# Optimization experiments

Hardware: AMD Instinct MI355X
Metric: run time of the kernel (lower is better)

The kernel has to match this reference:

```python
import jax, jax.numpy as jnp
import numpy as np

# ---- pywt filter banks (dec_lo, dec_hi, rec_lo, rec_hi), all pywt-ordered ----
_SQ2 = 0.7071067811865476

def _orth(dec_lo):
    dec_lo = np.asarray(dec_lo, dtype=np.float64)
    rec_lo = dec_lo[::-1].copy()
    k = np.arange(len(dec_lo))
    dec_hi = ((-1.0) ** (k + 1)) * rec_lo
    rec_hi = dec_hi[::-1].copy()
    return dec_lo, dec_hi, rec_lo, rec_hi

_DB4 = [-0.010597401784997278, 0.032883011666982945, 0.030841381835986965,
        -0.18703481171888114, -0.02798376941698385, 0.6308807679295904,
        0.7148465705525415, 0.23037781330885523]
_SYM6 = [-0.007800708325034148, 0.0017677118642428036, 0.04472490177066578,
         -0.021060292512300564, -0.07263752278646252, 0.3379294217276218,
         0.787641141030194, 0.4910559419267466, -0.048311742585633,
         -0.11799011114819057, 0.0034907120842174702, 0.015404109327027373]
_BIOR13 = (
    np.array([-0.08838834764831845, 0.08838834764831845, _SQ2, _SQ2, 0.08838834764831845, -0.08838834764831845]),
    np.array([0.0, 0.0, -_SQ2, _SQ2, 0.0, 0.0]),
    np.array([0.0, 0.0, _SQ2, _SQ2, 0.0, 0.0]),
    np.array([-0.08838834764831845, -0.08838834764831845, _SQ2, -_SQ2, 0.08838834764831845, 0.08838834764831845]),
)

WAVELETS = ['haar', 'db4', 'sym6', 'bior1.3']
FILTERS = {
    'haar': _orth([_SQ2, _SQ2]),
    'db4': _orth(_DB4),
    'sym6': _orth(_SYM6),
    'bior1.3': _BIOR13,
}
FILTERS = {k: tuple(jnp.asarray(f, dtype=jnp.float32) for f in v) for k, v in FILTERS.items()}


def _dwt(x, dec_lo, dec_hi):
    # x: [B, C, T] (T even). ptwt: reflect-pad (2L-3)//2 each side, stride-2 corr with flipped dec filters.
    B, C, T = x.shape
    L = dec_lo.shape[0]
    p = (2 * L - 3) // 2
    xp = jnp.pad(x, ((0, 0), (0, 0), (p, p)), mode='reflect') if p > 0 else x
    filt = jnp.stack([dec_lo[::-1], dec_hi[::-1]])[:, None, :].astype(x.dtype)  # [2,1,L]
    out = jax.lax.conv_general_dilated(
        xp.reshape(B * C, 1, -1), filt, window_strides=(2,), padding='VALID',
        dimension_numbers=('NCH', 'OIH', 'NCH'))
    out = out.reshape(B, C, 2, -1)
    return out[:, :, 0], out[:, :, 1]  # approx, detail: [B, C, (T+L-2)//2]


def _idwt(lo, hi, rec_lo, rec_hi):
    # conv_transpose stride 2 with rec filters, then crop (2L-3)//2 per side (ptwt waverec).
    B, C, Tc = lo.shape
    L = rec_lo.shape[0]
    p = (2 * L - 3) // 2
    c = jnp.stack([lo, hi], axis=2).reshape(B * C, 2, Tc)
    filt = jnp.stack([rec_lo[::-1], rec_hi[::-1]])[None].astype(lo.dtype)  # [1,2,L]
    y = jax.lax.conv_general_dilated(
        c, filt, window_strides=(1,), padding=[(L - 1, L - 1)],
        lhs_dilation=(2,), dimension_numbers=('NCH', 'OIH', 'NCH'))
    y = y.reshape(B, C, -1)
    if p > 0:
        y = y[:, :, p:-p]
    return y


def _spectral(z, lam, gamma, cos_theta):
    return gamma * jnp.sign(z) * jax.nn.relu(jnp.abs(z) - lam) * cos_theta


def setup_inputs() -> dict:
    key = jax.random.key(0)
    ks = jax.random.split(key, 8)
    B, S, E = 8, 4096, 1024
    x = jax.random.normal(ks[0], (B, S, E), dtype=jnp.float32)
    lambda_approx = jnp.full((1, E, 1), 0.05, jnp.float32) + 0.01 * jax.random.uniform(ks[1], (1, E, 1), jnp.float32)
    lambda_detail = jnp.full((1, E, 1), 0.05, jnp.float32) + 0.01 * jax.random.uniform(ks[2], (1, E, 1), jnp.float32)
    log_gamma = 0.1 * jax.random.normal(ks[3], (1, E, 1), jnp.float32)
    theta = 0.1 * jax.random.normal(ks[4], (1, E, 1), jnp.float32)
    basis_logits = 0.5 * jax.random.normal(ks[5], (4,), jnp.float32)
    ln_weight = jnp.ones((E,), jnp.float32)
    ln_bias = jnp.zeros((E,), jnp.float32)
    return {'x': x, 'lambda_approx': lambda_approx, 'lambda_detail': lambda_detail,
            'log_gamma': log_gamma, 'theta': theta, 'basis_logits': basis_logits,
            'ln_weight': ln_weight, 'ln_bias': ln_bias}


def reference(x, lambda_approx, lambda_detail, log_gamma, theta, basis_logits, ln_weight, ln_bias):
    residual = x                       # [B, S, E]
    S = x.shape[1]
    xt = jnp.transpose(x, (0, 2, 1))   # [B, E, S]
    gamma = jax.nn.softplus(log_gamma) + 1e-6
    ct = jnp.cos(theta)
    weights = jax.nn.softmax(basis_logits)  # all 4 wavelets valid for even S
    out = jnp.zeros_like(xt)
    for i, name in enumerate(WAVELETS):
        dl, dh, rl, rh = FILTERS[name]
        lo, hi = _dwt(xt, dl, dh)
        lo = _spectral(lo, lambda_approx, gamma, ct)
        hi = _spectral(hi, lambda_detail, gamma, ct)
        rec = _idwt(lo, hi, rl, rh)[:, :, :S]
        out = out + weights[i] * rec
    y = jnp.transpose(out, (0, 2, 1)) + residual
    mu = jnp.mean(y, axis=-1, keepdims=True)
    var = jnp.var(y, axis=-1, keepdims=True)
    return (y - mu) / jnp.sqrt(var + 1e-5) * ln_weight + ln_bias
```

## Files before the change

### kernel.cpp

```cpp
#include <hip/hip_runtime.h>
#include <cstdint>

#define T_SEQ 4096
#define E_DIM 1024
#define N_B   8
#define SC    64
typedef float v2f __attribute__((ext_vector_type(2)));

constexpr int LW[4] = {2, 8, 12, 6};

constexpr float DLf[4][12] = {
  {0.7071067811865476f, 0.7071067811865476f, 0,0,0,0,0,0,0,0,0,0},
  {-0.010597401784997278f, 0.032883011666982945f, 0.030841381835986965f, -0.18703481171888114f,
   -0.02798376941698385f, 0.6308807679295904f, 0.7148465705525415f, 0.23037781330885523f, 0,0,0,0},
  {-0.007800708325034148f, 0.0017677118642428036f, 0.04472490177066578f, -0.021060292512300564f,
   -0.07263752278646252f, 0.3379294217276218f, 0.787641141030194f, 0.4910559419267466f,
   -0.048311742585633f, -0.11799011114819057f, 0.0034907120842174702f, 0.015404109327027373f},
  {-0.08838834764831845f, 0.08838834764831845f, 0.7071067811865476f, 0.7071067811865476f,
    0.08838834764831845f, -0.08838834764831845f, 0,0,0,0,0,0},
};
constexpr float DHf[4][12] = {
  {-0.7071067811865476f, 0.7071067811865476f, 0,0,0,0,0,0,0,0,0,0},
  {-0.23037781330885523f, 0.7148465705525415f, -0.6308807679295904f, -0.02798376941698385f,
    0.18703481171888114f, 0.030841381835986965f, -0.032883011666982945f, -0.010597401784997278f, 0,0,0,0},
  {-0.015404109327027373f, 0.0034907120842174702f, 0.11799011114819057f, -0.048311742585633f,
   -0.4910559419267466f, 0.787641141030194f, -0.3379294217276218f, -0.07263752278646252f,
    0.021060292512300564f, 0.04472490177066578f, -0.0017677118642428036f, -0.007800708325034148f},
  {0,0,-0.7071067811865476f, 0.7071067811865476f, 0,0, 0,0,0,0,0,0},
};
constexpr float RLf[4][12] = {
  {0.7071067811865476f, 0.7071067811865476f, 0,0,0,0,0,0,0,0,0,0},
  {0.23037781330885523f, 0.7148465705525415f, 0.6308807679295904f, -0.02798376941698385f,
   -0.18703481171888114f, 0.030841381835986965f, 0.032883011666982945f, -0.010597401784997278f, 0,0,0,0},
  {0.015404109327027373f, 0.0034907120842174702f, -0.11799011114819057f, -0.048311742585633f,
   0.4910559419267466f, 0.787641141030194f, 0.3379294217276218f, -0.07263752278646252f,
   -0.021060292512300564f, 0.04472490177066578f, 0.0017677118642428036f, -0.007800708325034148f},
  {0,0,0.7071067811865476f, 0.7071067811865476f, 0,0, 0,0,0,0,0,0},
};
constexpr float RHf[4][12] = {
  {0.7071067811865476f, -0.7071067811865476f, 0,0,0,0,0,0,0,0,0,0},
  {-0.010597401784997278f, -0.032883011666982945f, 0.030841381835986965f, 0.18703481171888114f,
   -0.02798376941698385f, -0.6308807679295904f, 0.7148465705525415f, -0.23037781330885523f, 0,0,0,0},
  {-0.007800708325034148f, -0.0017677118642428036f, 0.04472490177066578f, 0.021060292512300564f,
   -0.07263752278646252f, -0.3379294217276218f, 0.787641141030194f, -0.4910559419267466f,
   -0.048311742585633f, 0.11799011114819057f, 0.0034907120842174702f, -0.015404109327027373f},
  {-0.08838834764831845f, -0.08838834764831845f, 0.7071067811865476f, -0.7071067811865476f,
    0.08838834764831845f, 0.08838834764831845f, 0,0,0,0,0,0},
};

__device__ __forceinline__ v2f sv(float c) { return v2f{c, c}; }

template <int W, int KK>
__device__ __forceinline__ void step(const v2f (&xw)[36], v2f (&acc)[16],
                                     const v2f la, const v2f ld, const v2f gw) {
  constexpr int L = LW[W];
  if constexpr (KK < L / 2 + 7) {
    v2f lo = {0.f, 0.f}, hi = {0.f, 0.f};
#pragma unroll
    for (int m = 0; m < L; ++m) {
      const v2f xv = xw[2 * KK + 11 - m];
      if (DLf[W][m] != 0.0f) lo += sv(DLf[W][m]) * xv;
      if (DHf[W][m] != 0.0f) hi += sv(DHf[W][m]) * xv;
    }
    v2f cl, ch;
    cl.x = __builtin_amdgcn_fmed3f(lo.x, -la.x, la.x);
    cl.y = __builtin_amdgcn_fmed3f(lo.y, -la.y, la.y);
    ch.x = __builtin_amdgcn_fmed3f(hi.x, -ld.x, ld.x);
    ch.y = __builtin_amdgcn_fmed3f(hi.y, -ld.y, ld.y);
    const v2f loS = (lo - cl) * gw;
    const v2f hiS = (hi - ch) * gw;
#pragma unroll
    for (int m = 0; m < L; ++m) {
      const int j = 2 * KK + m + 2 - L;
      if (j >= 0 && j < 16) {
        if (RLf[W][m] != 0.0f) acc[j] += loS * sv(RLf[W][m]);
        if (RHf[W][m] != 0.0f) acc[j] += hiS * sv(RHf[W][m]);
      }
    }
  }
}

template <int KK>
__device__ __forceinline__ void sweep(const v2f (&xw)[36], v2f (&acc)[16],
                                      const v2f la, const v2f ld,
                                      const v2f gw0, const v2f gw1,
                                      const v2f gw2, const v2f gw3) {
  if constexpr (KK < 13) {
    step<0, KK>(xw, acc, la, ld, gw0);
    step<1, KK>(xw, acc, la, ld, gw1);
    step<2, KK>(xw, acc, la, ld, gw2);
    step<3, KK>(xw, acc, la, ld, gw3);
    if constexpr (KK < 8) {
      acc[2 * KK]     += xw[2 * KK + 10];
      acc[2 * KK + 1] += xw[2 * KK + 11];
    }
    sweep<KK + 1>(xw, acc, la, ld, gw0, gw1, gw2, gw3);
  }
}

__global__ __launch_bounds__(256) void wlm_k1(
    const float* __restrict__ x,
    const float* __restrict__ la_, const float* __restrict__ ld_,
    const float* __restrict__ lg_, const float* __restrict__ th_,
    const float* __restrict__ bl_, float* __restrict__ y) {
  const int tid  = threadIdx.x;
  const int lane = tid & 63;
  const int wave = tid >> 6;
  const int s0 = blockIdx.x * SC;
  const int e0 = blockIdx.y * 128;
  const int b  = blockIdx.z;
  const int e  = e0 + 2 * lane;
  const int sA = s0 + wave * 16;

  const size_t rowb = (size_t)b * T_SEQ;
  v2f xw[36];
  if (sA >= 10 && sA + 26 <= T_SEQ) {
    const float* p = &x[(rowb + sA - 10) * E_DIM + e];
#pragma unroll
    for (int i = 0; i < 36; ++i) {
      xw[i] = *reinterpret_cast<const v2f*>(p + (size_t)i * E_DIM);
    }
  } else {
#pragma unroll
    for (int i = 0; i < 36; ++i) {
      int g = sA - 10 + i;
      g = (g < 0) ? -g : g;
      g = (g >= T_SEQ) ? (2 * T_SEQ - 2 - g) : g;
      xw[i] = *reinterpret_cast<const v2f*>(&x[(rowb + g) * E_DIM + e]);
    }
  }

  const v2f la = *reinterpret_cast<const v2f*>(&la_[e]);
  const v2f ld = *reinterpret_cast<const v2f*>(&ld_[e]);
  const v2f lg = *reinterpret_cast<const v2f*>(&lg_[e]);
  const v2f th = *reinterpret_cast<const v2f*>(&th_[e]);
  v2f g2;
  g2.x = (fmaxf(lg.x, 0.f) + log1pf(expf(-fabsf(lg.x))) + 1e-6f) * cosf(th.x);
  g2.y = (fmaxf(lg.y, 0.f) + log1pf(expf(-fabsf(lg.y))) + 1e-6f) * cosf(th.y);

  const float b0 = bl_[0], b1 = bl_[1], b2 = bl_[2], b3 = bl_[3];
  const float mx = fmaxf(fmaxf(b0, b1), fmaxf(b2, b3));
  const float w0 = expf(b0 - mx), w1 = expf(b1 - mx),
              w2 = expf(b2 - mx), w3 = expf(b3 - mx);
  const float wr = 1.f / (w0 + w1 + w2 + w3);
  const v2f gw0 = g2 * sv(w0 * wr), gw1 = g2 * sv(w1 * wr),
            gw2 = g2 * sv(w2 * wr), gw3 = g2 * sv(w3 * wr);

  v2f acc[16];
#pragma unroll
  for (int j = 0; j < 16; ++j) acc[j] = v2f{0.f, 0.f};

  sweep<0>(xw, acc, la, ld, gw0, gw1, gw2, gw3);

#pragma unroll
  for (int j = 0; j < 16; ++j) {
    *reinterpret_cast<v2f*>(&y[(rowb + sA + j) * E_DIM + e]) = acc[j];
  }
}

__global__ __launch_bounds__(256) void wlm_k2(float* __restrict__ y,
                                              const float* __restrict__ w,
                                              const float* __restrict__ bias) {
  const int token = blockIdx.x;
  const int tid = threadIdx.x;
  float* row = y + (size_t)token * E_DIM;

  float4 v = *reinterpret_cast<const float4*>(&row[tid * 4]);
  float s  = v.x + v.y + v.z + v.w;
  float sq = v.x * v.x + v.y * v.y + v.z * v.z + v.w * v.w;
#pragma unroll
  for (int off = 32; off; off >>= 1) {
    s  += __shfl_down(s, off);
    sq += __shfl_down(sq, off);
  }
  __shared__ float ps[4], pq[4], stat[2];
  const int wave = tid >> 6, lane = tid & 63;
  if (lane == 0) { ps[wave] = s; pq[wave] = sq; }
  __syncthreads();
  if (tid == 0) {
    const float S1 = ps[0] + ps[1] + ps[2] + ps[3];
    const float S2 = pq[0] + pq[1] + pq[2] + pq[3];
    const float mu = S1 * (1.f / E_DIM);
    const float var = S2 * (1.f / E_DIM) - mu * mu;
    stat[0] = mu;
    stat[1] = rsqrtf(var + 1e-5f);
  }
  __syncthreads();
  const float mu = stat[0], rstd = stat[1];
  const float4 wv = *reinterpret_cast<const float4*>(&w[tid * 4]);
  const float4 bv = *reinterpret_cast<const float4*>(&bias[tid * 4]);
  float4 o;
  o.x = (v.x - mu) * rstd * wv.x + bv.x;
  o.y = (v.y - mu) * rstd * wv.y + bv.y;
  o.z = (v.z - mu) * rstd * wv.z + bv.z;
  o.w = (v.w - mu) * rstd * wv.w + bv.w;
  *reinterpret_cast<float4*>(&row[tid * 4]) = o;
}

extern "C" void kernel_launch(void* const* d_in, const int* in_sizes, int n_in,
                              void* d_out, int out_size, void* d_ws, size_t ws_size,
                              hipStream_t stream) {
  const float* x   = (const float*)d_in[0];
  const float* la  = (const float*)d_in[1];
  const float* ldt = (const float*)d_in[2];
  const float* lg  = (const float*)d_in[3];
  const float* th  = (const float*)d_in[4];
  const float* bl  = (const float*)d_in[5];
  const float* lnw = (const float*)d_in[6];
  const float* lnb = (const float*)d_in[7];
  float* out = (float*)d_out;

  dim3 g1(T_SEQ / SC, E_DIM / 128, N_B);
  wlm_k1<<<g1, 256, 0, stream>>>(x, la, ldt, lg, th, bl, out);
  wlm_k2<<<dim3(N_B * T_SEQ), 256, 0, stream>>>(out, lnw, lnb);
}
```

Baseline: 111.9 us.

## Fuse wavelet filtering and LayerNorm into one kernel with full-row blocks

Merges the wavelet filter kernel and the LayerNorm kernel into a single kernel. Each 512-thread block now covers all 1024 channels for 16 consecutive tokens, so per-row mean and variance are reduced in-block through shuffles and shared memory. This removes the intermediate write and re-read of the full output tensor and one kernel launch. In exchange, the grid shrinks to 2048 blocks, the x halo is re-read per 16-token tile, and 16 serial per-row reductions are added per thread.

```diff
diff --git a/kernel.cpp b/kernel.cpp
--- a/kernel.cpp
+++ b/kernel.cpp
@@ -4,7 +4,7 @@
 #define T_SEQ 4096
 #define E_DIM 1024
 #define N_B   8
-#define SC    64
+#define BT    16
 typedef float v2f __attribute__((ext_vector_type(2)));
 
 constexpr int LW[4] = {2, 8, 12, 6};
@@ -98,19 +98,21 @@
   }
 }
 
-__global__ __launch_bounds__(256) void wlm_k1(
+__global__ __launch_bounds__(512) void wlm_fused(
     const float* __restrict__ x,
     const float* __restrict__ la_, const float* __restrict__ ld_,
     const float* __restrict__ lg_, const float* __restrict__ th_,
-    const float* __restrict__ bl_, float* __restrict__ y) {
+    const float* __restrict__ bl_,
+    const float* __restrict__ lnw, const float* __restrict__ lnb,
+    float* __restrict__ y) {
+  __shared__ float ps[BT][8], pq[BT][8], stat[BT][2];
+
   const int tid  = threadIdx.x;
   const int lane = tid & 63;
   const int wave = tid >> 6;
-  const int s0 = blockIdx.x * SC;
-  const int e0 = blockIdx.y * 128;
+  const int e  = 2 * tid;
   const int b  = blockIdx.z;
-  const int e  = e0 + 2 * lane;
-  const int sA = s0 + wave * 16;
+  const int sA = blockIdx.x * BT;
 
   const size_t rowb = (size_t)b * T_SEQ;
   v2f xw[36];
@@ -153,48 +155,36 @@
   sweep<0>(xw, acc, la, ld, gw0, gw1, gw2, gw3);
 
 #pragma unroll
-  for (int j = 0; j < 16; ++j) {
-    *reinterpret_cast<v2f*>(&y[(rowb + sA + j) * E_DIM + e]) = acc[j];
-  }
-}
-
-__global__ __launch_bounds__(256) void wlm_k2(float* __restrict__ y,
-                                              const float* __restrict__ w,
-                                              const float* __restrict__ bias) {
-  const int token = blockIdx.x;
-  const int tid = threadIdx.x;
-  float* row = y + (size_t)token * E_DIM;
-
-  float4 v = *reinterpret_cast<const float4*>(&row[tid * 4]);
-  float s  = v.x + v.y + v.z + v.w;
-  float sq = v.x * v.x + v.y * v.y + v.z * v.z + v.w * v.w;
-#pragma unroll
-  for (int off = 32; off; off >>= 1) {
-    s  += __shfl_down(s, off);
-    sq += __shfl_down(sq, off);
-  }
-  __shared__ float ps[4], pq[4], stat[2];
-  const int wave = tid >> 6, lane = tid & 63;
-  if (lane == 0) { ps[wave] = s; pq[wave] = sq; }
+  for (int j = 0; j < BT; ++j) {
+    float s = acc[j].x + acc[j].y;
+    float q = acc[j].x * acc[j].x + acc[j].y * acc[j].y;
+#pragma unroll
+    for (int off = 32; off; off >>= 1) {
+      s += __shfl_down(s, off);
+      q += __shfl_down(q, off);
+    }
+    if (lane == 0) { ps[j][wave] = s; pq[j][wave] = q; }
+  }
   __syncthreads();
-  if (tid == 0) {
-    const float S1 = ps[0] + ps[1] + ps[2] + ps[3];
-    const float S2 = pq[0] + pq[1] + pq[2] + pq[3];
-    const float mu = S1 * (1.f / E_DIM);
-    const float var = S2 * (1.f / E_DIM) - mu * mu;
-    stat[0] = mu;
-    stat[1] = rsqrtf(var + 1e-5f);
+  if (tid < BT) {
+    float S = 0.f, Q = 0.f;
+#pragma unroll
+    for (int w = 0; w < 8; ++w) { S += ps[tid][w]; Q += pq[tid][w]; }
+    const float mu = S * (1.f / E_DIM);
+    const float var = Q * (1.f / E_DIM) - mu * mu;
+    stat[tid][0] = mu;
+    stat[tid][1] = rsqrtf(var + 1e-5f);
   }
   __syncthreads();
-  const float mu = stat[0], rstd = stat[1];
-  const float4 wv = *reinterpret_cast<const float4*>(&w[tid * 4]);
-  const float4 bv = *reinterpret_cast<const float4*>(&bias[tid * 4]);
-  float4 o;
-  o.x = (v.x - mu) * rstd * wv.x + bv.x;
-  o.y = (v.y - mu) * rstd * wv.y + bv.y;
-  o.z = (v.z - mu) * rstd * wv.z + bv.z;
-  o.w = (v.w - mu) * rstd * wv.w + bv.w;
-  *reinterpret_cast<float4*>(&row[tid * 4]) = o;
+
+  const v2f wv = *reinterpret_cast<const v2f*>(&lnw[e]);
+  const v2f bv = *reinterpret_cast<const v2f*>(&lnb[e]);
+#pragma unroll
+  for (int j = 0; j < BT; ++j) {
+    const float mu = stat[j][0], rs = stat[j][1];
+    const v2f o = (acc[j] - sv(mu)) * sv(rs) * wv + bv;
+    *reinterpret_cast<v2f*>(&y[(rowb + sA + j) * E_DIM + e]) = o;
+  }
 }
 
 extern "C" void kernel_launch(void* const* d_in, const int* in_sizes, int n_in,
@@ -210,7 +200,6 @@
   const float* lnb = (const float*)d_in[7];
   float* out = (float*)d_out;
 
-  dim3 g1(T_SEQ / SC, E_DIM / 128, N_B);
-  wlm_k1<<<g1, 256, 0, stream>>>(x, la, ldt, lg, th, bl, out);
-  wlm_k2<<<dim3(N_B * T_SEQ), 256, 0, stream>>>(out, lnw, lnb);
-}
+  dim3 g(T_SEQ / BT, 1, N_B);
+  wlm_fused<<<g, 512, 0, stream>>>(x, la, ldt, lg, th, bl, lnw, lnb, out);
+}
```

New measurement: 137.9 us. 1.23x slower.

## Stage input tile with halo in LDS via direct global-to-LDS loads

Applied to the files above, without the earlier changes.

Each block now loads a 148-row by 64-channel tile of x, including the reflect halo, into shared memory using global_load_lds, then each thread reads its 36-row window from LDS. This replaces per-wave redundant global reads of overlapping halos. The tile shape changes to 128 sequence positions by 64 channels, and an occupancy hint is added. It relies on correct waiting for the async LDS loads before the barrier.

```diff
diff --git a/kernel.cpp b/kernel.cpp
--- a/kernel.cpp
+++ b/kernel.cpp
@@ -4,7 +4,8 @@
 #define T_SEQ 4096
 #define E_DIM 1024
 #define N_B   8
-#define SC    64
+#define SC    128
+#define TILE_P 148
 typedef float v2f __attribute__((ext_vector_type(2)));
 
 constexpr int LW[4] = {2, 8, 12, 6};
@@ -98,38 +99,48 @@
   }
 }
 
-__global__ __launch_bounds__(256) void wlm_k1(
+__device__ __forceinline__ void gload_lds16(const float* gsrc, float* ldst) {
+  __builtin_amdgcn_global_load_lds(
+      (const __attribute__((address_space(1))) void*)gsrc,
+      (__attribute__((address_space(3))) void*)ldst, 16, 0, 0);
+}
+
+__global__ __launch_bounds__(256)
+__attribute__((amdgpu_waves_per_eu(4)))
+void wlm_k1(
     const float* __restrict__ x,
     const float* __restrict__ la_, const float* __restrict__ ld_,
     const float* __restrict__ lg_, const float* __restrict__ th_,
     const float* __restrict__ bl_, float* __restrict__ y) {
+  __shared__ float xs[TILE_P][64];
+
   const int tid  = threadIdx.x;
   const int lane = tid & 63;
   const int wave = tid >> 6;
   const int s0 = blockIdx.x * SC;
-  const int e0 = blockIdx.y * 128;
+  const int e0 = blockIdx.y * 64;
   const int b  = blockIdx.z;
-  const int e  = e0 + 2 * lane;
-  const int sA = s0 + wave * 16;
-
   const size_t rowb = (size_t)b * T_SEQ;
-  v2f xw[36];
-  if (sA >= 10 && sA + 26 <= T_SEQ) {
-    const float* p = &x[(rowb + sA - 10) * E_DIM + e];
-#pragma unroll
-    for (int i = 0; i < 36; ++i) {
-      xw[i] = *reinterpret_cast<const v2f*>(p + (size_t)i * E_DIM);
-    }
-  } else {
-#pragma unroll
-    for (int i = 0; i < 36; ++i) {
-      int g = sA - 10 + i;
-      g = (g < 0) ? -g : g;
-      g = (g >= T_SEQ) ? (2 * T_SEQ - 2 - g) : g;
-      xw[i] = *reinterpret_cast<const v2f*>(&x[(rowb + g) * E_DIM + e]);
-    }
-  }
-
+
+  {
+    const int ch4  = (lane & 15) * 4;
+    const int psub = lane >> 4;
+#pragma unroll
+    for (int it = 0; it < 10; ++it) {
+      const int rg = wave + it * 4;
+      if (rg < TILE_P / 4) {
+        const int pos = rg * 4 + psub;
+        int g = s0 - 10 + pos;
+        g = (g < 0) ? -g : g;
+        g = (g >= T_SEQ) ? (2 * T_SEQ - 2 - g) : g;
+        gload_lds16(&x[(rowb + g) * E_DIM + e0 + ch4], &xs[rg * 4][0]);
+      }
+    }
+  }
+
+  const int c  = tid & 31;
+  const int pg = tid >> 5;
+  const int e  = e0 + 2 * c;
   const v2f la = *reinterpret_cast<const v2f*>(&la_[e]);
   const v2f ld = *reinterpret_cast<const v2f*>(&ld_[e]);
   const v2f lg = *reinterpret_cast<const v2f*>(&lg_[e]);
@@ -146,12 +157,21 @@
   const v2f gw0 = g2 * sv(w0 * wr), gw1 = g2 * sv(w1 * wr),
             gw2 = g2 * sv(w2 * wr), gw3 = g2 * sv(w3 * wr);
 
+  __syncthreads();
+
+  v2f xw[36];
+#pragma unroll
+  for (int i = 0; i < 36; ++i) {
+    xw[i] = *reinterpret_cast<const v2f*>(&xs[pg * 16 + i][2 * c]);
+  }
+
   v2f acc[16];
 #pragma unroll
   for (int j = 0; j < 16; ++j) acc[j] = v2f{0.f, 0.f};
 
   sweep<0>(xw, acc, la, ld, gw0, gw1, gw2, gw3);
 
+  const int sA = s0 + pg * 16;
 #pragma unroll
   for (int j = 0; j < 16; ++j) {
     *reinterpret_cast<v2f*>(&y[(rowb + sA + j) * E_DIM + e]) = acc[j];
@@ -210,7 +230,7 @@
   const float* lnb = (const float*)d_in[7];
   float* out = (float*)d_out;
 
-  dim3 g1(T_SEQ / SC, E_DIM / 128, N_B);
+  dim3 g1(T_SEQ / SC, E_DIM / 64, N_B);
   wlm_k1<<<g1, 256, 0, stream>>>(x, la, ldt, lg, th, bl, out);
   wlm_k2<<<dim3(N_B * T_SEQ), 256, 0, stream>>>(out, lnw, lnb);
 }
```

After: 111.0 us. Within noise of the previous version (-0.7%).
